# Performance work log

Measured on AMD Instinct MI355X. Metric: run time of the kernel, lower is better.

## Reference

```python
import jax, jax.numpy as jnp
import numpy as np

B, T, V, S = 32, 2048, 1024, 256
BLANK = 0
NEG = -1e30  # log-space 'zero' (avoids inf so zero_infinity handling is a simple threshold)


def setup_inputs() -> dict:
    key = jax.random.key(0)
    k1, k2, k3, k4 = jax.random.split(key, 4)
    # valid log-probabilities, as produced by an upstream log_softmax head
    preds_logprob = jax.nn.log_softmax(
        jax.random.normal(k1, (B, T, V), dtype=jnp.float32), axis=-1)
    tokens_gt = jax.random.randint(k2, (B, S), 1, V)            # labels exclude blank=0
    cqt_lens = jax.random.randint(k3, (B,), T // 2, T + 1)      # input lengths
    token_lens_gt = jax.random.randint(k4, (B,), S // 2, S + 1) # target lengths (>=1)
    return {"preds_logprob": preds_logprob, "tokens_gt": tokens_gt,
            "cqt_lens": cqt_lens, "token_lens_gt": token_lens_gt}


def _ctc_single(lp, ext, rep_ok, Tl, Sl):
    """Negative CTC log-likelihood for one sample.
    lp: [T, V] log-probs; ext: [L=2S+1] extended label seq (blanks interleaved);
    rep_ok: [L] bool, whether the s-2 -> s skip transition is allowed;
    Tl: input length; Sl: target length (>=1)."""
    emit = lp[:, ext]  # [T, L] emission log-probs, gathered once outside the scan
    L = ext.shape[0]
    alpha = jnp.full((L,), NEG, dtype=lp.dtype)
    alpha = alpha.at[0].set(emit[0, 0]).at[1].set(emit[0, 1])

    neg1 = jnp.full((1,), NEG, dtype=lp.dtype)
    neg2 = jnp.full((2,), NEG, dtype=lp.dtype)

    def step(alpha, xs):
        e, t = xs
        a1 = jnp.concatenate([neg1, alpha[:-1]])
        a2 = jnp.concatenate([neg2, alpha[:-2]])
        a2 = jnp.where(rep_ok, a2, NEG)
        m = jnp.maximum(jnp.maximum(alpha, a1), a2)
        new = e + m + jnp.log(jnp.exp(alpha - m) + jnp.exp(a1 - m) + jnp.exp(a2 - m))
        # freeze the lattice past this sample's input length (masking by cqt_lens)
        alpha = jnp.where(t < Tl, new, alpha)
        return alpha, None

    ts = jnp.arange(1, lp.shape[0])
    alpha, _ = jax.lax.scan(step, alpha, (emit[1:], ts))

    # log-likelihood = logsumexp over the two terminal lattice states
    lA = alpha[2 * Sl]
    lB = alpha[2 * Sl - 1]
    m = jnp.maximum(lA, lB)
    ll = m + jnp.log(jnp.exp(lA - m) + jnp.exp(lB - m))
    return -ll


def _ctc_loss(preds_logprob, tokens_gt, cqt_lens, token_lens_gt):
    # mask_by_length: zero out frames past cqt_lens (no effect on CTC value,
    # kept for faithfulness); swapaxes(0,1) is a pure layout change.
    tmask = jnp.arange(T)[None, :] < cqt_lens[:, None]          # [B, T]
    lp = preds_logprob * tmask[:, :, None].astype(preds_logprob.dtype)

    # extended label sequence with blanks interleaved: [blank, y1, blank, ..., yS, blank]
    ext = jnp.zeros((B, 2 * S + 1), dtype=tokens_gt.dtype).at[:, 1::2].set(tokens_gt)
    ext_m2 = jnp.concatenate([jnp.zeros((B, 2), dtype=ext.dtype), ext[:, :-2]], axis=1)
    rep_ok = (ext != BLANK) & (ext != ext_m2)                   # allow s-2 skip

    losses = jax.vmap(_ctc_single)(lp, ext, rep_ok, cqt_lens, token_lens_gt)  # [B]
    # zero_infinity=True: unreachable alignments produce ~ -NEG; zero them out
    losses = jnp.where(losses > 1e29, 0.0, losses)
    # reduction='mean': divide by target length, then mean over batch
    return jnp.mean(losses / token_lens_gt.astype(losses.dtype))


def reference(preds_logprob, tokens_gt, cqt_lens, token_lens_gt):
    return _ctc_loss(preds_logprob, tokens_gt, cqt_lens, token_lens_gt)
```

## Files before the change

### kernel.cpp

```cpp
#include <hip/hip_runtime.h>
#include <math.h>

#define BB 32
#define TT 2048
#define VV 1024
#define SS 256
#define TCHUNK 4

__device__ __forceinline__ void async_ld16(const float* g, const float* l) {
    __builtin_amdgcn_global_load_lds(
        (const __attribute__((address_space(1))) void*)(uintptr_t)g,
        (__attribute__((address_space(3))) void*)(unsigned)(uintptr_t)l, 16, 0, 0);
}
__device__ __forceinline__ void async_ld4(const float* g, const float* l) {
    __builtin_amdgcn_global_load_lds(
        (const __attribute__((address_space(1))) void*)(uintptr_t)g,
        (__attribute__((address_space(3))) void*)(unsigned)(uintptr_t)l, 4, 0, 0);
}
#define WAIT_VM27() __builtin_amdgcn_s_waitcnt(0x4F7B)
#define WAIT_VM18() __builtin_amdgcn_s_waitcnt(0x4F72)
#define WAIT_VM0()  __builtin_amdgcn_s_waitcnt(0x0F70)

__device__ __forceinline__ float dpp_shr1_f(float x) {
    int r = __builtin_amdgcn_update_dpp(0, __float_as_int(x), 0x138, 0xF, 0xF, true);
    return __int_as_float(r);
}
__device__ __forceinline__ int dpp_shr1_i(int x) {
    return __builtin_amdgcn_update_dpp(0, x, 0x138, 0xF, 0xF, true);
}

__global__ __launch_bounds__(256) void ctc_pre(const float* __restrict__ lp,
    const int* __restrict__ tokens, const int* __restrict__ cqt,
    const int* __restrict__ slen, float* __restrict__ G, float* __restrict__ Gbl,
    float* __restrict__ out)
{
    __shared__ __align__(16) float rows[TCHUNK][VV];
    __shared__ int toks[SS];
    const int tid = threadIdx.x;
    const int bx  = blockIdx.x;
    if (bx == 0 && tid == 0) out[0] = 0.f;
    const int nchunk = TT / TCHUNK;
    const int b  = bx / nchunk;
    const int t0 = (bx % nchunk) * TCHUNK;
    const int Tl = cqt[b];
    if (t0 >= Tl) return;
    const int Sl = slen[b];
    toks[tid] = tokens[b * SS + tid];
#pragma unroll
    for (int k = 0; k < TCHUNK; ++k) {
        const int t = t0 + k;
        if (t < Tl)
            ((float4*)rows[k])[tid] = ((const float4*)(lp + ((size_t)b * TT + t) * VV))[tid];
    }
    __syncthreads();
#pragma unroll
    for (int k = 0; k < TCHUNK; ++k) {
        const int t = t0 + k;
        if (t >= Tl) break;
        float* gp = G + ((size_t)b * TT + t) * 256;
        gp[tid] = (tid < Sl) ? __expf(rows[k][toks[tid]]) : 0.f;
        if (tid == 0) Gbl[b * TT + t] = __expf(rows[k][0]);
    }
}

__global__ __launch_bounds__(64) void ctc_walk(const float* __restrict__ G,
    const float* __restrict__ Gbl, const int* __restrict__ tokens,
    const int* __restrict__ cqt, const int* __restrict__ slen, float* __restrict__ out)
{
    __shared__ __align__(16) float tokL[4][8 * 256];
    __shared__ __align__(16) float blkL[4][64];
    __shared__ float als[513];
    __shared__ int   aE[65];

    const int b    = blockIdx.x;
    const int lane = threadIdx.x;
    const int Tl   = cqt[b];
    const int Sl   = slen[b];
    const float* __restrict__ Gb   = G   + (size_t)b * TT * 256;
    const float* __restrict__ GblB = Gbl + (size_t)b * TT;
    const int j0 = lane * 4;
    const int* tb = tokens + b * SS;
    const int tm1 = (j0 == 0) ? 0 : tb[j0 - 1];
    const int q0 = tb[j0], q1 = tb[j0 + 1], q2 = tb[j0 + 2], q3 = tb[j0 + 3];
    const float m0 = (q0 != tm1) ? 1.f : 0.f;
    const float m1 = (q1 != q0)  ? 1.f : 0.f;
    const float m2 = (q2 != q1)  ? 1.f : 0.f;
    const float m3 = (q3 != q2)  ? 1.f : 0.f;
    const float lzm = (lane == 0) ? 0.f : 1.f;

    float a0=0.f,a1=0.f,a2=0.f,a3=0.f,a4=0.f,a5=0.f,a6=0.f,a7=0.f,aX=0.f;
    if (lane == 0) { a0 = GblB[0]; a1 = Gb[0]; }
    int   Etot = 0;
    float sfac = lzm;

#define ISSUE(slot, tbase) do { \
    const float* lt = tokL[slot]; \
    _Pragma("unroll") \
    for (int k = 0; k < 8; ++k) { \
        int tt = (tbase) + k; tt = (tt < Tl) ? tt : (Tl - 1); \
        async_ld16(Gb + (size_t)tt * 256 + (lane << 2), lt + k * 256); \
    } \
    int tbk = (tbase) + lane; tbk = (tbk < Tl) ? tbk : (Tl - 1); \
    async_ld4(GblB + tbk, blkL[slot]); \
} while (0)

#define LOADCHUNK(s) do { \
    _Pragma("unroll") \
    for (int k = 0; k < 8; ++k) { \
        pr[k] = ((const float4*)(tokL[s] + (k << 8)))[lane]; \
        pb[k] = blkL[s][k]; \
    } \
} while (0)

#define ONESTEP(P4, PB) do { \
    const float pb_ = (PB); \
    const float h1 = dpp_shr1_f(a7) * sfac; \
    const float n0 = pb_ * (a0 + h1); \
    const float n1 = (P4).x * (a1 + a0 + m0 * h1); \
    const float n2 = pb_ * (a2 + a1); \
    const float n3 = (P4).y * (a3 + a2 + m1 * a1); \
    const float n4 = pb_ * (a4 + a3); \
    const float n5 = (P4).z * (a5 + a4 + m2 * a3); \
    const float n6 = pb_ * (a6 + a5); \
    const float n7 = (P4).w * (a7 + a6 + m3 * a5); \
    aX = pb_ * (aX + a7); \
    a0=n0;a1=n1;a2=n2;a3=n3;a4=n4;a5=n5;a6=n6;a7=n7; \
} while (0)

#define RENORM_LOCAL() do { \
    float mm = fmaxf(fmaxf(fmaxf(a0,a1),fmaxf(a2,a3)), fmaxf(fmaxf(a4,a5),fmaxf(a6,a7))); \
    mm = fmaxf(mm, aX); \
    int ee = (__float_as_int(mm) >> 23) - 126; \
    ee = (mm > 0.f) ? ee : 0; \
    const float sc = __int_as_float((127 - ee) << 23); \
    a0*=sc;a1*=sc;a2*=sc;a3*=sc;a4*=sc;a5*=sc;a6*=sc;a7*=sc;aX*=sc; \
    Etot += ee; \
    int Ep = dpp_shr1_i(Etot); \
    if (mm == 0.f && lane > 0) Etot = Ep; \
    Ep = dpp_shr1_i(Etot); \
    if (mm == 0.f && lane > 0) Etot = Ep; \
    int dd = Ep - Etot; \
    dd = (dd < -126) ? -126 : ((dd > 100) ? 100 : dd); \
    sfac = __int_as_float((127 + dd) << 23) * lzm; \
} while (0)

    float4 pr[8];
    float  pb[8];

    ISSUE(0, 1); ISSUE(1, 9); ISSUE(2, 17);
    int t = 1, slot = 0;
    while (t + 8 <= Tl) {
        const int ns = (slot + 3) & 3;
        ISSUE(ns, t + 24);
        WAIT_VM27();
        __builtin_amdgcn_sched_barrier(0);
        LOADCHUNK(slot);
#pragma unroll
        for (int k = 0; k < 8; ++k) {
            ONESTEP(pr[k], pb[k]);
            if (k == 3 || k == 7) RENORM_LOCAL();
        }
        t += 8; slot = (slot + 1) & 3;
    }
    if (t < Tl) {
        WAIT_VM18();
        __builtin_amdgcn_sched_barrier(0);
        LOADCHUNK(slot);
        const int nv = Tl - t;
#pragma unroll
        for (int k = 0; k < 8; ++k) {
            if (k < nv) ONESTEP(pr[k], pb[k]);
            if (k == 3 || k == 7) RENORM_LOCAL();
        }
    }
    WAIT_VM0();

    als[8 * lane + 0] = a0; als[8 * lane + 1] = a1;
    als[8 * lane + 2] = a2; als[8 * lane + 3] = a3;
    als[8 * lane + 4] = a4; als[8 * lane + 5] = a5;
    als[8 * lane + 6] = a6; als[8 * lane + 7] = a7;
    aE[lane] = Etot;
    if (lane == 63) { als[512] = aX; aE[64] = Etot; }
    __syncthreads();
    if (lane == 0) {
        const int sA = 2 * Sl, sB = 2 * Sl - 1;
        const float vA = als[sA], vB = als[sB];
        const int   eA = aE[sA >> 3], eB = aE[sB >> 3];
        int em;
        if (vA > 0.f && vB > 0.f) em = (eA > eB) ? eA : eB;
        else if (vA > 0.f)        em = eA;
        else if (vB > 0.f)        em = eB;
        else                      em = 0;
        const double s = ldexp((double)vA, eA - em) + ldexp((double)vB, eB - em);
        double loss = -(log(s) + (double)em * 0.6931471805599453);
        if (!(loss < 1e29)) loss = 0.0;
        atomicAdd(out, (float)(loss / ((double)Sl * (double)BB)));
    }
#undef ISSUE
#undef LOADCHUNK
#undef ONESTEP
#undef RENORM_LOCAL
}

extern "C" void kernel_launch(void* const* d_in, const int* in_sizes, int n_in,
                              void* d_out, int out_size, void* d_ws, size_t ws_size,
                              hipStream_t stream)
{
    const float* lp     = (const float*)d_in[0];
    const int*   tokens = (const int*)d_in[1];
    const int*   cqt    = (const int*)d_in[2];
    const int*   slen   = (const int*)d_in[3];
    float* out = (float*)d_out;
    float* G   = (float*)d_ws;
    float* Gbl = G + (size_t)BB * TT * 256;

    hipLaunchKernelGGL(ctc_pre,  dim3(BB * (TT / TCHUNK)), dim3(256), 0, stream,
                       lp, tokens, cqt, slen, G, Gbl, out);
    hipLaunchKernelGGL(ctc_walk, dim3(BB), dim3(64), 0, stream,
                       G, Gbl, tokens, cqt, slen, out);
}
```

Baseline: 542.9 us.

## Warp-specialize CTC walk: producer wavefronts prefetch emissions into LDS ring buffer

The walk kernel now runs four wavefronts per sample. Three producer wavefronts issue async global-to-LDS loads into a six-slot ring and publish readiness flags in shared memory. The single consumer wavefront spins on those flags and runs the recurrence, so it no longer issues loads or waits on vmcnt itself. This takes memory latency off the serial critical path, at the cost of spin-wait synchronisation through volatile LDS flags and possible ordering hazards.

Measured after the change: 519.1 us. -4.4%, faster.

```diff
diff --git a/kernel.cpp b/kernel.cpp
--- a/kernel.cpp
+++ b/kernel.cpp
@@ -6,6 +6,7 @@
 #define VV 1024
 #define SS 256
 #define TCHUNK 4
+#define NSLOT 6
 
 __device__ __forceinline__ void async_ld16(const float* g, const float* l) {
     __builtin_amdgcn_global_load_lds(
@@ -17,9 +18,7 @@
         (const __attribute__((address_space(1))) void*)(uintptr_t)g,
         (__attribute__((address_space(3))) void*)(unsigned)(uintptr_t)l, 4, 0, 0);
 }
-#define WAIT_VM27() __builtin_amdgcn_s_waitcnt(0x4F7B)
-#define WAIT_VM18() __builtin_amdgcn_s_waitcnt(0x4F72)
-#define WAIT_VM0()  __builtin_amdgcn_s_waitcnt(0x0F70)
+#define WAIT_VM0() __builtin_amdgcn_s_waitcnt(0x0F70)
 
 __device__ __forceinline__ float dpp_shr1_f(float x) {
     int r = __builtin_amdgcn_update_dpp(0, __float_as_int(x), 0x138, 0xF, 0xF, true);
@@ -63,21 +62,57 @@
     }
 }
 
-__global__ __launch_bounds__(64) void ctc_walk(const float* __restrict__ G,
+__global__ __launch_bounds__(256) void ctc_walk(const float* __restrict__ G,
     const float* __restrict__ Gbl, const int* __restrict__ tokens,
     const int* __restrict__ cqt, const int* __restrict__ slen, float* __restrict__ out)
 {
-    __shared__ __align__(16) float tokL[4][8 * 256];
-    __shared__ __align__(16) float blkL[4][64];
+    __shared__ __align__(16) float tokL[NSLOT][8 * 256];
+    __shared__ __align__(16) float blkL[NSLOT][64];
     __shared__ float als[513];
     __shared__ int   aE[65];
+    __shared__ int   ready[NSLOT];
+    __shared__ int   prog;
 
     const int b    = blockIdx.x;
-    const int lane = threadIdx.x;
+    const int tid  = threadIdx.x;
+    const int wid  = tid >> 6;
+    const int lane = tid & 63;
     const int Tl   = cqt[b];
-    const int Sl   = slen[b];
     const float* __restrict__ Gb   = G   + (size_t)b * TT * 256;
     const float* __restrict__ GblB = Gbl + (size_t)b * TT;
+
+    if (tid < NSLOT) ready[tid] = -1;
+    if (tid == NSLOT) prog = -1;
+    __syncthreads();
+
+    const int NC = (Tl + 6) >> 3;
+    volatile int* vready = ready;
+    volatile int* vprog  = &prog;
+
+    if (wid != 0) {
+        for (int c = wid - 1; c < NC; c += 3) {
+            const int slot = c % NSLOT;
+            while (*vprog < c - NSLOT) {}
+            __builtin_amdgcn_sched_barrier(0);
+            asm volatile("" ::: "memory");
+            const int tbase = 1 + (c << 3);
+            const float* lt = tokL[slot];
+#pragma unroll
+            for (int k = 0; k < 8; ++k) {
+                int tt = tbase + k; tt = (tt < Tl) ? tt : (Tl - 1);
+                async_ld16(Gb + (size_t)tt * 256 + (lane << 2), lt + k * 256);
+            }
+            int tbk = tbase + lane; tbk = (tbk < Tl) ? tbk : (Tl - 1);
+            async_ld4(GblB + tbk, blkL[slot]);
+            WAIT_VM0();
+            __builtin_amdgcn_sched_barrier(0);
+            asm volatile("" ::: "memory");
+            vready[slot] = c;
+        }
+        return;
+    }
+
+    const int Sl = slen[b];
     const int j0 = lane * 4;
     const int* tb = tokens + b * SS;
     const int tm1 = (j0 == 0) ? 0 : tb[j0 - 1];
@@ -92,17 +127,6 @@
     if (lane == 0) { a0 = GblB[0]; a1 = Gb[0]; }
     int   Etot = 0;
     float sfac = lzm;
-
-#define ISSUE(slot, tbase) do { \
-    const float* lt = tokL[slot]; \
-    _Pragma("unroll") \
-    for (int k = 0; k < 8; ++k) { \
-        int tt = (tbase) + k; tt = (tt < Tl) ? tt : (Tl - 1); \
-        async_ld16(Gb + (size_t)tt * 256 + (lane << 2), lt + k * 256); \
-    } \
-    int tbk = (tbase) + lane; tbk = (tbk < Tl) ? tbk : (Tl - 1); \
-    async_ld4(GblB + tbk, blkL[slot]); \
-} while (0)
 
 #define LOADCHUNK(s) do { \
     _Pragma("unroll") \
@@ -147,33 +171,36 @@
     float4 pr[8];
     float  pb[8];
 
-    ISSUE(0, 1); ISSUE(1, 9); ISSUE(2, 17);
-    int t = 1, slot = 0;
-    while (t + 8 <= Tl) {
-        const int ns = (slot + 3) & 3;
-        ISSUE(ns, t + 24);
-        WAIT_VM27();
+    const int F = (Tl - 1) >> 3;
+    for (int c = 0; c < F; ++c) {
+        const int slot = c % NSLOT;
+        while (vready[slot] < c) {}
         __builtin_amdgcn_sched_barrier(0);
+        asm volatile("" ::: "memory");
         LOADCHUNK(slot);
+        asm volatile("" ::: "memory");
+        *vprog = c;
 #pragma unroll
         for (int k = 0; k < 8; ++k) {
             ONESTEP(pr[k], pb[k]);
             if (k == 3 || k == 7) RENORM_LOCAL();
         }
-        t += 8; slot = (slot + 1) & 3;
-    }
-    if (t < Tl) {
-        WAIT_VM18();
+    }
+    if (F < NC) {
+        const int slot = F % NSLOT;
+        while (vready[slot] < F) {}
         __builtin_amdgcn_sched_barrier(0);
+        asm volatile("" ::: "memory");
         LOADCHUNK(slot);
-        const int nv = Tl - t;
+        asm volatile("" ::: "memory");
+        *vprog = F;
+        const int nv = (Tl - 1) - (F << 3);
 #pragma unroll
         for (int k = 0; k < 8; ++k) {
             if (k < nv) ONESTEP(pr[k], pb[k]);
             if (k == 3 || k == 7) RENORM_LOCAL();
         }
     }
-    WAIT_VM0();
 
     als[8 * lane + 0] = a0; als[8 * lane + 1] = a1;
     als[8 * lane + 2] = a2; als[8 * lane + 3] = a3;
@@ -181,7 +208,7 @@
     als[8 * lane + 6] = a6; als[8 * lane + 7] = a7;
     aE[lane] = Etot;
     if (lane == 63) { als[512] = aX; aE[64] = Etot; }
-    __syncthreads();
+    asm volatile("s_waitcnt lgkmcnt(0)" ::: "memory");
     if (lane == 0) {
         const int sA = 2 * Sl, sB = 2 * Sl - 1;
         const float vA = als[sA], vB = als[sB];
@@ -196,7 +223,6 @@
         if (!(loss < 1e29)) loss = 0.0;
         atomicAdd(out, (float)(loss / ((double)Sl * (double)BB)));
     }
-#undef ISSUE
 #undef LOADCHUNK
 #undef ONESTEP
 #undef RENORM_LOCAL
@@ -216,6 +242,6 @@
 
     hipLaunchKernelGGL(ctc_pre,  dim3(BB * (TT / TCHUNK)), dim3(256), 0, stream,
                        lp, tokens, cqt, slen, G, Gbl, out);
-    hipLaunchKernelGGL(ctc_walk, dim3(BB), dim3(64), 0, stream,
+    hipLaunchKernelGGL(ctc_walk, dim3(BB), dim3(256), 0, stream,
                        G, Gbl, tokens, cqt, slen, out);
 }
```
